# Kernel tuning notes

Measured on AMD Instinct MI355X. Metric: run time of the kernel, lower is better.

The kernel has to match this reference:

```python
import jax, jax.numpy as jnp
import numpy as np
from jax import lax

B, D, N = 1024, 1024, 65536
M, Ks, DS = 8, 256, 128      # key PQ: subvectors, codewords, subvec dim (D/M)
MV, DV = 8, 256              # value PQ: subvectors, subvec dim (OUT/MV)
OUT = MV * DV
K_TOP = 64


def setup_inputs() -> dict:
    key = jax.random.key(0)
    ks = jax.random.split(key, 7)
    x = jax.random.normal(ks[0], (B, D), dtype=jnp.float32)
    # whitening matrix starts as identity in the module; perturb slightly for a non-trivial test
    whitening_matrix = jnp.eye(D, dtype=jnp.float32) + 0.01 * jax.random.normal(ks[1], (D, D), dtype=jnp.float32)
    key_codebooks = jax.random.normal(ks[2], (M, Ks, DS), dtype=jnp.float32)
    value_codebooks = jax.random.normal(ks[3], (MV, Ks, DV), dtype=jnp.float32)
    bias = jnp.zeros((OUT,), dtype=jnp.float32)
    key_codes = jax.random.randint(ks[4], (N, M), 0, Ks, dtype=jnp.int32)
    value_codes = jax.random.randint(ks[5], (N, MV), 0, Ks, dtype=jnp.int32)
    return {
        "x": x,
        "whitening_matrix": whitening_matrix,
        "key_codebooks": key_codebooks,
        "value_codebooks": value_codebooks,
        "bias": bias,
        "key_codes": key_codes,
        "value_codes": value_codes,
        "k": K_TOP,
    }


def reference(x, whitening_matrix, key_codebooks, value_codebooks, bias, key_codes, value_codes, k):
    # 1) whiten the query (module buffer 'whitening_matrix')
    q = x @ whitening_matrix                      # [B, D]
    qs = q.reshape(B, M, DS)                      # [B, M, DS] query subvectors

    # 2) ADC distance tables: squared L2 between each query subvector and each codeword
    #    dt[b, m, c] = ||qs[b,m] - cb[m,c]||^2
    q_sq = jnp.sum(qs * qs, axis=-1)              # [B, M]
    c_sq = jnp.sum(key_codebooks * key_codebooks, axis=-1)  # [M, Ks]
    cross = jnp.einsum("bmd,mcd->bmc", qs, key_codebooks)   # [B, M, Ks]
    dt = q_sq[:, :, None] + c_sq[None, :, :] - 2.0 * cross  # [B, M, Ks]

    # 3) asymmetric distance to all N stored keys via code gather (irregular access)
    lut = dt.transpose(1, 0, 2)                   # [M, B, Ks]
    # per-subvector gather then sum: d[b, n] = sum_m lut[m, b, key_codes[n, m]]
    dists = jax.vmap(lambda l, c: l[:, c])(lut, key_codes.T).sum(axis=0)  # [B, N]

    # 4) top-k nearest neighbors
    neg_top, top_idx = lax.top_k(-dists, k)       # [B, k]

    # 5) reconstruct values of retrieved neighbors from value PQ codebooks
    vc = value_codes[top_idx]                     # [B, k, MV] int codes
    vals = value_codebooks[jnp.arange(MV)[None, None, :], vc]  # [B, k, MV, DV]
    vals = vals.reshape(vals.shape[0], vals.shape[1], OUT)      # [B, k, OUT]

    # 6) distance-weighted aggregation (softmax over negative distances) + bias
    w = jax.nn.softmax(neg_top, axis=-1)          # [B, k]
    y = jnp.einsum("bk,bko->bo", w, vals) + bias  # [B, OUT]
    return y
```

## Files before the change

### kernel.cpp

```cpp
#include <hip/hip_runtime.h>

#define N_ITEMS 65536

__launch_bounds__(256)
__global__ void gemm_q_kernel(const float* __restrict__ A,
                              const float* __restrict__ W,
                              float* __restrict__ qpart) {
  __shared__ float As[16][132];
  __shared__ float Bs[16][132];
  const int tid = threadIdx.x;
  const int tx = tid & 15, ty = tid >> 4;
  const int rb = blockIdx.y * 128, cb = blockIdx.x * 128;
  const int kz = blockIdx.z * 256;
  const int ar = tid >> 2, ac = (tid & 3) << 2;
  const int bk = tid >> 5, bc = (tid & 31) << 2;

  float4 va0 = *(const float4*)&A[(rb + ar) * 1024 + kz + ac];
  float4 va1 = *(const float4*)&A[(rb + ar + 64) * 1024 + kz + ac];
  float4 vb0 = *(const float4*)&W[(kz + bk) * 1024 + cb + bc];
  float4 vb1 = *(const float4*)&W[(kz + bk + 8) * 1024 + cb + bc];

  float acc[8][8] = {};
  for (int k0 = 0; k0 < 256; k0 += 16) {
    As[ac + 0][ar] = va0.x; As[ac + 1][ar] = va0.y;
    As[ac + 2][ar] = va0.z; As[ac + 3][ar] = va0.w;
    As[ac + 0][ar + 64] = va1.x; As[ac + 1][ar + 64] = va1.y;
    As[ac + 2][ar + 64] = va1.z; As[ac + 3][ar + 64] = va1.w;
    *(float4*)&Bs[bk][bc] = vb0;
    *(float4*)&Bs[bk + 8][bc] = vb1;
    __syncthreads();
    if (k0 + 16 < 256) {
      va0 = *(const float4*)&A[(rb + ar) * 1024 + kz + k0 + 16 + ac];
      va1 = *(const float4*)&A[(rb + ar + 64) * 1024 + kz + k0 + 16 + ac];
      vb0 = *(const float4*)&W[(kz + k0 + 16 + bk) * 1024 + cb + bc];
      vb1 = *(const float4*)&W[(kz + k0 + 16 + bk + 8) * 1024 + cb + bc];
    }
#pragma unroll
    for (int kk = 0; kk < 16; kk++) {
      const float4 a0 = *(const float4*)&As[kk][ty << 2];
      const float4 a1 = *(const float4*)&As[kk][64 + (ty << 2)];
      const float4 b0 = *(const float4*)&Bs[kk][tx << 2];
      const float4 b1 = *(const float4*)&Bs[kk][64 + (tx << 2)];
      const float ar8[8] = {a0.x, a0.y, a0.z, a0.w, a1.x, a1.y, a1.z, a1.w};
      const float br8[8] = {b0.x, b0.y, b0.z, b0.w, b1.x, b1.y, b1.z, b1.w};
#pragma unroll
      for (int r = 0; r < 8; r++)
#pragma unroll
        for (int c = 0; c < 8; c++)
          acc[r][c] = fmaf(ar8[r], br8[c], acc[r][c]);
    }
    __syncthreads();
  }
  float* outp = qpart + blockIdx.z * 1048576;
#pragma unroll
  for (int rh = 0; rh < 2; rh++)
#pragma unroll
    for (int r = 0; r < 4; r++) {
      const int row = rb + rh * 64 + (ty << 2) + r;
      const int ri = rh * 4 + r;
      *(float4*)&outp[row * 1024 + cb + (tx << 2)] =
          make_float4(acc[ri][0], acc[ri][1], acc[ri][2], acc[ri][3]);
      *(float4*)&outp[row * 1024 + cb + 64 + (tx << 2)] =
          make_float4(acc[ri][4], acc[ri][5], acc[ri][6], acc[ri][7]);
    }
}

__launch_bounds__(256)
__global__ void lut_kernel(const float* __restrict__ qpart,
                           const float* __restrict__ kcb,
                           const int* __restrict__ key_codes,
                           float* __restrict__ lut,
                           unsigned long long* __restrict__ pcodes,
                           uint4* __restrict__ poffs) {
  if (blockIdx.z == 8) {
    const int g0 = (((int)blockIdx.y * 4 + (int)blockIdx.x) * 256 + (int)threadIdx.x) * 4;
#pragma unroll
    for (int t = 0; t < 4; t++) {
      const int gid = g0 + t;
      unsigned long long p = 0ull;
      unsigned h[8];
#pragma unroll
      for (int j = 0; j < 8; j++) {
        const unsigned c = (unsigned)key_codes[gid * 8 + j] & 255u;
        p |= (unsigned long long)c << (8 * j);
        h[j] = ((c >> 1) << 7) | ((c & 1u) << 2);
      }
      pcodes[gid] = p;
      poffs[gid] = make_uint4(h[0] | (h[1] << 16), h[2] | (h[3] << 16),
                              h[4] | (h[5] << 16), h[6] | (h[7] << 16));
    }
    return;
  }

  __shared__ float As[32][68];
  __shared__ float Bs[32][68];
  const int tid = threadIdx.x;
  const int tx = tid & 15, ty = tid >> 4;
  const int m = blockIdx.z;
  const int rb = blockIdx.y * 64;
  const int cb0 = blockIdx.x * 64;
  float acc[4][4] = {};
  float qa[4] = {}, cs[4] = {};
  for (int k0 = 0; k0 < 128; k0 += 32) {
#pragma unroll
    for (int l = 0; l < 2; l++) {
      const int e = tid + l * 256;
      const int row = e >> 3, c4 = (e & 7) << 2;
      const int qidx = (rb + row) * 1024 + m * 128 + k0 + c4;
      const float4 p0 = *(const float4*)&qpart[qidx];
      const float4 p1 = *(const float4*)&qpart[qidx + 1048576];
      const float4 p2 = *(const float4*)&qpart[qidx + 2097152];
      const float4 p3 = *(const float4*)&qpart[qidx + 3145728];
      const float4 va = make_float4(p0.x + p1.x + p2.x + p3.x,
                                    p0.y + p1.y + p2.y + p3.y,
                                    p0.z + p1.z + p2.z + p3.z,
                                    p0.w + p1.w + p2.w + p3.w);
      As[c4 + 0][row] = va.x; As[c4 + 1][row] = va.y;
      As[c4 + 2][row] = va.z; As[c4 + 3][row] = va.w;
      const float4 vb = *(const float4*)&kcb[(m * 256 + cb0 + row) * 128 + k0 + c4];
      Bs[c4 + 0][row] = vb.x; Bs[c4 + 1][row] = vb.y;
      Bs[c4 + 2][row] = vb.z; Bs[c4 + 3][row] = vb.w;
    }
    __syncthreads();
#pragma unroll
    for (int kk = 0; kk < 32; kk++) {
      const float4 a = *(const float4*)&As[kk][ty << 2];
      const float4 b = *(const float4*)&Bs[kk][tx << 2];
      const float ar[4] = {a.x, a.y, a.z, a.w};
      const float br[4] = {b.x, b.y, b.z, b.w};
#pragma unroll
      for (int r = 0; r < 4; r++)
#pragma unroll
        for (int c = 0; c < 4; c++)
          acc[r][c] = fmaf(ar[r], br[c], acc[r][c]);
#pragma unroll
      for (int r = 0; r < 4; r++) qa[r] = fmaf(ar[r], ar[r], qa[r]);
#pragma unroll
      for (int c = 0; c < 4; c++) cs[c] = fmaf(br[c], br[c], cs[c]);
    }
    __syncthreads();
  }
#pragma unroll
  for (int r = 0; r < 4; r++) {
    const int row = rb + (ty << 2) + r;
    const int col = cb0 + (tx << 2);
    float4 v;
    v.x = qa[r] + cs[0] - 2.0f * acc[r][0];
    v.y = qa[r] + cs[1] - 2.0f * acc[r][1];
    v.z = qa[r] + cs[2] - 2.0f * acc[r][2];
    v.w = qa[r] + cs[3] - 2.0f * acc[r][3];
    *(float4*)&lut[row * 2048 + m * 256 + col] = v;
  }
}

extern __shared__ char dyn_lds[];

__launch_bounds__(1024)
__global__ void scan2r_kernel(const float* __restrict__ lut,
                              const uint4* __restrict__ poffs,
                              unsigned* __restrict__ cand_d,
                              unsigned short* __restrict__ cand_n) {
  char* repb = dyn_lds;
  unsigned* repw = (unsigned*)dyn_lds;
  short* temps = (short*)(dyn_lds + 131072);
  unsigned* tempw = (unsigned*)(dyn_lds + 131072);
  const int tid = threadIdx.x;
  const int g = blockIdx.x;

  {
    const int w = tid >> 6, lane = tid & 63;
    const int rr = w & 1, seg = w >> 1;
    const int row = (g << 1) + rr;
    const int e0 = seg * 256 + lane * 4;
    const float4 v4 = *(const float4*)&lut[row * 2048 + e0];
    float s4 = v4.x + v4.y + v4.z + v4.w;
#pragma unroll
    for (int off = 32; off > 0; off >>= 1) s4 += __shfl_xor(s4, off);
    const float mean = s4 * (1.0f / 256.0f);
    const float vals[4] = {v4.x, v4.y, v4.z, v4.w};
#pragma unroll
    for (int k = 0; k < 4; k++) {
      float f = (vals[k] - mean) * 64.0f;
      f = fmaxf(fminf(f, 32000.0f), -32000.0f);
      temps[(e0 + k) * 2 + rr] = (short)(int)rintf(f);
    }
  }
  __syncthreads();

  {
    const int lane = tid & 63;
    const unsigned v0 = tempw[tid * 2];
    const unsigned v1 = tempw[tid * 2 + 1];
    const int Dbase = tid * 32;
#pragma unroll
    for (int k = 0; k < 16; k++) {
      const int r = (k + lane) & 15;
      repw[Dbase + 2 * r] = v0;
      repw[Dbase + 1 + 2 * r] = v1;
    }
  }
  __syncthreads();

  const int r = tid & 15;
  const char* base0 = repb + (r << 3);
  const char* base1 = repb + 65536 + (r << 3);
  int d0a = 0x7FFFFFFF, d1a = 0x7FFFFFFF, i0a = 0, i1a = 0;
  int d0b = 0x7FFFFFFF, d1b = 0x7FFFFFFF, i0b = 0, i1b = 0;

  uint4 oc = poffs[tid];
  uint4 nc = poffs[tid + 1024];
  for (int it = 0; it < 64; it++) {
    const int n = tid + (it << 10);
    uint4 nn2 = nc;
    if (it < 62) nn2 = poffs[n + 2048];
    unsigned wv;
    int s0, s1;
    wv = *(const unsigned*)(base0 + (oc.x & 0xFFFFu));
    s0 = (int)(short)wv; s1 = ((int)wv) >> 16;
#define LK(B, HV, OFS) { wv = *(const unsigned*)((B) + (HV) + (OFS)); \
    s0 += (int)(short)wv; s1 += ((int)wv) >> 16; }
    LK(base0, oc.x >> 16, 16384)
    LK(base0, oc.y & 0xFFFFu, 32768)
    LK(base0, oc.y >> 16, 49152)
    LK(base1, oc.z & 0xFFFFu, 0)
    LK(base1, oc.z >> 16, 16384)
    LK(base1, oc.w & 0xFFFFu, 32768)
    LK(base1, oc.w >> 16, 49152)
#undef LK
    if (s0 < d1a) {
      if (s0 < d0a) { d1a = d0a; i1a = i0a; d0a = s0; i0a = n; }
      else          { d1a = s0; i1a = n; }
    }
    if (s1 < d1b) {
      if (s1 < d0b) { d1b = d0b; i1b = i0b; d0b = s1; i0b = n; }
      else          { d1b = s1; i1b = n; }
    }
    oc = nc; nc = nn2;
  }

  {
    const int ba = (g << 1) * 2048 + tid * 2;
    *(uint2*)&cand_d[ba] = make_uint2((unsigned)(d0a + 0x40000000),
                                      (unsigned)(d1a + 0x40000000));
    *(unsigned*)&cand_n[ba] = (unsigned)i0a | ((unsigned)i1a << 16);
    const int bb = ((g << 1) + 1) * 2048 + tid * 2;
    *(uint2*)&cand_d[bb] = make_uint2((unsigned)(d0b + 0x40000000),
                                      (unsigned)(d1b + 0x40000000));
    *(unsigned*)&cand_n[bb] = (unsigned)i0b | ((unsigned)i1b << 16);
  }
}

__launch_bounds__(512)
__global__ void scan16_kernel(const float* __restrict__ lut,
                              const unsigned long long* __restrict__ pcodes,
                              unsigned* __restrict__ cand_d,
                              unsigned short* __restrict__ cand_n) {
  __shared__ short sRep[32768];
  const int tid = threadIdx.x;
  const int b = blockIdx.x;

  const float4 v4 = *(const float4*)&lut[b * 2048 + tid * 4];
  float s4 = v4.x + v4.y + v4.z + v4.w;
#pragma unroll
  for (int off = 32; off > 0; off >>= 1) s4 += __shfl_xor(s4, off);
  const float mean = s4 * (1.0f / 256.0f);

  const float vals[4] = {v4.x, v4.y, v4.z, v4.w};
#pragma unroll
  for (int k2 = 0; k2 < 4; k2++) {
    float f = (vals[k2] - mean) * 64.0f;
    f = fmaxf(fminf(f, 32000.0f), -32000.0f);
    const int iv = (int)rintf(f);
    const unsigned hw = (unsigned)(unsigned short)iv;
    const unsigned wrd = hw | (hw << 16);
    const uint4 wv = make_uint4(wrd, wrd, wrd, wrd);
    const int e = tid * 4 + k2;
    *(uint4*)&((unsigned*)sRep)[e * 8] = wv;
    *(uint4*)&((unsigned*)sRep)[e * 8 + 4] = wv;
  }
  __syncthreads();

  const int r = tid & 15;
  int d0 = 0x7FFFFFFF, d1 = 0x7FFFFFFF, d2 = 0x7FFFFFFF, d3 = 0x7FFFFFFF;
  int i0 = 0, i1 = 0, i2 = 0, i3 = 0;

  unsigned long long c8 = pcodes[tid];
  for (int it = 0; it < 128; it++) {
    const int n = tid + (it << 9);
    unsigned long long nxt = 0ull;
    if (it < 127) nxt = pcodes[n + 512];
    const unsigned lo = (unsigned)c8;
    const unsigned hi = (unsigned)(c8 >> 32);
    int s;
    s  = sRep[(((lo      ) & 255u) << 4) + r        ];
    s += sRep[(((lo >>  8) & 255u) << 4) + r +  4096];
    s += sRep[(((lo >> 16) & 255u) << 4) + r +  8192];
    s += sRep[(((lo >> 24)       ) << 4) + r + 12288];
    s += sRep[(((hi      ) & 255u) << 4) + r + 16384];
    s += sRep[(((hi >>  8) & 255u) << 4) + r + 20480];
    s += sRep[(((hi >> 16) & 255u) << 4) + r + 24576];
    s += sRep[(((hi >> 24)       ) << 4) + r + 28672];
    if (s < d3) {
      if (s < d1) {
        if (s < d0) { d3 = d2; i3 = i2; d2 = d1; i2 = i1; d1 = d0; i1 = i0; d0 = s; i0 = n; }
        else        { d3 = d2; i3 = i2; d2 = d1; i2 = i1; d1 = s; i1 = n; }
      } else {
        if (s < d2) { d3 = d2; i3 = i2; d2 = s; i2 = n; }
        else        { d3 = s; i3 = n; }
      }
    }
    c8 = nxt;
  }

  const int base = b * 2048 + tid * 4;
  const uint4 dv = make_uint4((unsigned)(d0 + 0x40000000), (unsigned)(d1 + 0x40000000),
                              (unsigned)(d2 + 0x40000000), (unsigned)(d3 + 0x40000000));
  *(uint4*)&cand_d[base] = dv;
  const unsigned ni01 = (unsigned)i0 | ((unsigned)i1 << 16);
  const unsigned ni23 = (unsigned)i2 | ((unsigned)i3 << 16);
  *(uint2*)&cand_n[base] = make_uint2(ni01, ni23);
}

__launch_bounds__(256)
__global__ void select_kernel(const unsigned* __restrict__ cand_d,
                              const unsigned short* __restrict__ cand_n,
                              const int* __restrict__ value_codes,
                              const float* __restrict__ vcb,
                              const float* __restrict__ bias,
                              float* __restrict__ out) {
  __shared__ unsigned sredw[4];
  __shared__ unsigned long long clist[256];
  __shared__ float sw[256];
  __shared__ int svc[2048];
  __shared__ int scnt;
  __shared__ float sWsum;

  const int tid = threadIdx.x;
  const int b = blockIdx.x;

  const uint4 a0 = *(const uint4*)&cand_d[b * 2048 + tid * 8];
  const uint4 a1 = *(const uint4*)&cand_d[b * 2048 + tid * 8 + 4];
  const uint4 nn = *(const uint4*)&cand_n[b * 2048 + tid * 8];
  unsigned dk[8] = {a0.x, a0.y, a0.z, a0.w, a1.x, a1.y, a1.z, a1.w};
  unsigned ni[8] = {nn.x & 0xFFFFu, nn.x >> 16, nn.y & 0xFFFFu, nn.y >> 16,
                    nn.z & 0xFFFFu, nn.z >> 16, nn.w & 0xFFFFu, nn.w >> 16};

  if (tid == 0) scnt = 0;
  unsigned mn = dk[0];
#pragma unroll
  for (int j = 1; j < 8; j++) mn = (dk[j] < mn) ? dk[j] : mn;
#pragma unroll
  for (int off = 32; off > 0; off >>= 1) {
    const unsigned o = __shfl_xor(mn, off);
    mn = (o < mn) ? o : mn;
  }
  if ((tid & 63) == 0) sredw[tid >> 6] = mn;
  __syncthreads();
  unsigned sMin = sredw[0];
  sMin = (sredw[1] < sMin) ? sredw[1] : sMin;
  sMin = (sredw[2] < sMin) ? sredw[2] : sMin;
  sMin = (sredw[3] < sMin) ? sredw[3] : sMin;
  const unsigned lim = sMin + 2048u;

  const int lane = tid & 63;
  const unsigned long long lm = (1ull << lane) - 1ull;
#pragma unroll
  for (int j = 0; j < 8; j++) {
    const bool pred = dk[j] <= lim;
    const unsigned long long mask = __ballot(pred);
    int base = 0;
    if (lane == 0 && mask) base = atomicAdd(&scnt, __popcll(mask));
    base = __shfl(base, 0);
    if (pred) {
      const int pos = base + __popcll(mask & lm);
      if (pos < 256) clist[pos] = ((unsigned long long)dk[j] << 32) | ni[j];
    }
  }
  __syncthreads();
  const int cnt = min(scnt, 256);

  if (tid < cnt) {
    const int gap = (int)((unsigned)(clist[tid] >> 32)) - (int)sMin;
    sw[tid] = __expf((float)gap * -0.015625f);
  }
  for (int i = tid; i < (cnt << 3); i += 256)
    svc[i] = value_codes[((int)(clist[i >> 3] & 0xFFFFFFFFu)) * 8 + (i & 7)];
  __syncthreads();

  if (tid < 64) {
    float s = 0.f;
    for (int j = tid; j < cnt; j += 64) s += sw[j];
#pragma unroll
    for (int off = 32; off > 0; off >>= 1) s += __shfl_xor(s, off);
    if (tid == 0) sWsum = s;
  }
  __syncthreads();
  const float inv = 1.0f / sWsum;

  const int c0 = tid << 3;
  const int mv = c0 >> 8;
  const int off = c0 & 255;
  float4 acc0 = make_float4(0.f, 0.f, 0.f, 0.f);
  float4 acc1 = make_float4(0.f, 0.f, 0.f, 0.f);
  const float* vbase = vcb + mv * 65536 + off;
  for (int k = 0; k < cnt; k++) {
    const float w = sw[k];
    const float* vp = vbase + svc[(k << 3) + mv] * 256;
    const float4 v0 = *(const float4*)vp;
    const float4 v1 = *(const float4*)(vp + 4);
    acc0.x = fmaf(w, v0.x, acc0.x); acc0.y = fmaf(w, v0.y, acc0.y);
    acc0.z = fmaf(w, v0.z, acc0.z); acc0.w = fmaf(w, v0.w, acc0.w);
    acc1.x = fmaf(w, v1.x, acc1.x); acc1.y = fmaf(w, v1.y, acc1.y);
    acc1.z = fmaf(w, v1.z, acc1.z); acc1.w = fmaf(w, v1.w, acc1.w);
  }
  const float4 b0 = *(const float4*)&bias[c0];
  const float4 b1 = *(const float4*)&bias[c0 + 4];
  *(float4*)&out[b * 2048 + c0] =
      make_float4(fmaf(acc0.x, inv, b0.x), fmaf(acc0.y, inv, b0.y),
                  fmaf(acc0.z, inv, b0.z), fmaf(acc0.w, inv, b0.w));
  *(float4*)&out[b * 2048 + c0 + 4] =
      make_float4(fmaf(acc1.x, inv, b1.x), fmaf(acc1.y, inv, b1.y),
                  fmaf(acc1.z, inv, b1.z), fmaf(acc1.w, inv, b1.w));
}

extern "C" void kernel_launch(void* const* d_in, const int* in_sizes, int n_in,
                              void* d_out, int out_size, void* d_ws, size_t ws_size,
                              hipStream_t stream) {
  const float* x    = (const float*)d_in[0];
  const float* W    = (const float*)d_in[1];
  const float* kcb  = (const float*)d_in[2];
  const float* vcb  = (const float*)d_in[3];
  const float* bias = (const float*)d_in[4];
  const int* key_codes   = (const int*)d_in[5];
  const int* value_codes = (const int*)d_in[6];
  float* out = (float*)d_out;

  float* qpart = (float*)d_ws;
  float* lut   = qpart + 4194304;
  uint4* poffs = (uint4*)(lut + 2097152);
  unsigned long long* pcodes = (unsigned long long*)(poffs + 65536);
  unsigned* cand_d = (unsigned*)d_ws;
  unsigned short* cand_n = (unsigned short*)(cand_d + 2097152);

  hipLaunchKernelGGL(gemm_q_kernel, dim3(8, 8, 4), dim3(256), 0, stream,
                     x, W, qpart);
  hipLaunchKernelGGL(lut_kernel, dim3(4, 16, 9), dim3(256), 0, stream,
                     qpart, kcb, key_codes, lut, pcodes, poffs);

  const hipError_t attr_rc = hipFuncSetAttribute(
      (const void*)scan2r_kernel, hipFuncAttributeMaxDynamicSharedMemorySize, 139264);
  if (attr_rc == hipSuccess) {
    hipLaunchKernelGGL(scan2r_kernel, dim3(512), dim3(1024), 139264, stream,
                       lut, poffs, cand_d, cand_n);
  } else {
    hipLaunchKernelGGL(scan16_kernel, dim3(1024), dim3(512), 0, stream,
                       lut, pcodes, cand_d, cand_n);
  }

  hipLaunchKernelGGL(select_kernel, dim3(1024), dim3(256), 0, stream,
                     cand_d, cand_n, value_codes, vcb, bias, out);
}
```

Before: 197.4 us.

## Shrink GEMM tiles to 64x64 single-wave blocks and move code packing into GEMM launch

The whitening GEMM now uses 64-thread blocks on 64x64 output tiles, so a 16x16x4 grid launches 1024 blocks instead of 256 to fill more compute units. The key-code packing work moves from the LUT kernel's extra z-slice into an extra z-slice of the GEMM launch, so it runs alongside the GEMM. The LUT kernel loses those blocks. Smaller tiles lower operand reuse per block and raise global and LDS traffic per flop.

```diff
diff --git a/kernel.cpp b/kernel.cpp
--- a/kernel.cpp
+++ b/kernel.cpp
@@ -2,78 +2,15 @@
 
 #define N_ITEMS 65536
 
-__launch_bounds__(256)
+__launch_bounds__(64)
 __global__ void gemm_q_kernel(const float* __restrict__ A,
                               const float* __restrict__ W,
-                              float* __restrict__ qpart) {
-  __shared__ float As[16][132];
-  __shared__ float Bs[16][132];
-  const int tid = threadIdx.x;
-  const int tx = tid & 15, ty = tid >> 4;
-  const int rb = blockIdx.y * 128, cb = blockIdx.x * 128;
-  const int kz = blockIdx.z * 256;
-  const int ar = tid >> 2, ac = (tid & 3) << 2;
-  const int bk = tid >> 5, bc = (tid & 31) << 2;
-
-  float4 va0 = *(const float4*)&A[(rb + ar) * 1024 + kz + ac];
-  float4 va1 = *(const float4*)&A[(rb + ar + 64) * 1024 + kz + ac];
-  float4 vb0 = *(const float4*)&W[(kz + bk) * 1024 + cb + bc];
-  float4 vb1 = *(const float4*)&W[(kz + bk + 8) * 1024 + cb + bc];
-
-  float acc[8][8] = {};
-  for (int k0 = 0; k0 < 256; k0 += 16) {
-    As[ac + 0][ar] = va0.x; As[ac + 1][ar] = va0.y;
-    As[ac + 2][ar] = va0.z; As[ac + 3][ar] = va0.w;
-    As[ac + 0][ar + 64] = va1.x; As[ac + 1][ar + 64] = va1.y;
-    As[ac + 2][ar + 64] = va1.z; As[ac + 3][ar + 64] = va1.w;
-    *(float4*)&Bs[bk][bc] = vb0;
-    *(float4*)&Bs[bk + 8][bc] = vb1;
-    __syncthreads();
-    if (k0 + 16 < 256) {
-      va0 = *(const float4*)&A[(rb + ar) * 1024 + kz + k0 + 16 + ac];
-      va1 = *(const float4*)&A[(rb + ar + 64) * 1024 + kz + k0 + 16 + ac];
-      vb0 = *(const float4*)&W[(kz + k0 + 16 + bk) * 1024 + cb + bc];
-      vb1 = *(const float4*)&W[(kz + k0 + 16 + bk + 8) * 1024 + cb + bc];
-    }
-#pragma unroll
-    for (int kk = 0; kk < 16; kk++) {
-      const float4 a0 = *(const float4*)&As[kk][ty << 2];
-      const float4 a1 = *(const float4*)&As[kk][64 + (ty << 2)];
-      const float4 b0 = *(const float4*)&Bs[kk][tx << 2];
-      const float4 b1 = *(const float4*)&Bs[kk][64 + (tx << 2)];
-      const float ar8[8] = {a0.x, a0.y, a0.z, a0.w, a1.x, a1.y, a1.z, a1.w};
-      const float br8[8] = {b0.x, b0.y, b0.z, b0.w, b1.x, b1.y, b1.z, b1.w};
-#pragma unroll
-      for (int r = 0; r < 8; r++)
-#pragma unroll
-        for (int c = 0; c < 8; c++)
-          acc[r][c] = fmaf(ar8[r], br8[c], acc[r][c]);
-    }
-    __syncthreads();
-  }
-  float* outp = qpart + blockIdx.z * 1048576;
-#pragma unroll
-  for (int rh = 0; rh < 2; rh++)
-#pragma unroll
-    for (int r = 0; r < 4; r++) {
-      const int row = rb + rh * 64 + (ty << 2) + r;
-      const int ri = rh * 4 + r;
-      *(float4*)&outp[row * 1024 + cb + (tx << 2)] =
-          make_float4(acc[ri][0], acc[ri][1], acc[ri][2], acc[ri][3]);
-      *(float4*)&outp[row * 1024 + cb + 64 + (tx << 2)] =
-          make_float4(acc[ri][4], acc[ri][5], acc[ri][6], acc[ri][7]);
-    }
-}
-
-__launch_bounds__(256)
-__global__ void lut_kernel(const float* __restrict__ qpart,
-                           const float* __restrict__ kcb,
-                           const int* __restrict__ key_codes,
-                           float* __restrict__ lut,
-                           unsigned long long* __restrict__ pcodes,
-                           uint4* __restrict__ poffs) {
-  if (blockIdx.z == 8) {
-    const int g0 = (((int)blockIdx.y * 4 + (int)blockIdx.x) * 256 + (int)threadIdx.x) * 4;
+                              float* __restrict__ qpart,
+                              const int* __restrict__ key_codes,
+                              unsigned long long* __restrict__ pcodes,
+                              uint4* __restrict__ poffs) {
+  if (blockIdx.z == 4) {
+    const int g0 = (((int)blockIdx.y * 16 + (int)blockIdx.x) * 64 + (int)threadIdx.x) * 4;
 #pragma unroll
     for (int t = 0; t < 4; t++) {
       const int gid = g0 + t;
@@ -92,6 +29,74 @@
     return;
   }
 
+  __shared__ float As[16][68];
+  __shared__ float Bs[16][68];
+  const int tid = threadIdx.x;
+  const int tx = tid & 7, ty = tid >> 3;
+  const int rb = blockIdx.y * 64, cb = blockIdx.x * 64;
+  const int kz = blockIdx.z * 256;
+
+  float4 va[4], vb[4];
+#pragma unroll
+  for (int j = 0; j < 4; j++) {
+    const int e = tid + (j << 6);
+    va[j] = *(const float4*)&A[(rb + (e >> 2)) * 1024 + kz + ((e & 3) << 2)];
+    vb[j] = *(const float4*)&W[(kz + (e >> 4)) * 1024 + cb + ((e & 15) << 2)];
+  }
+
+  float acc[8][8] = {};
+  for (int k0 = 0; k0 < 256; k0 += 16) {
+#pragma unroll
+    for (int j = 0; j < 4; j++) {
+      const int e = tid + (j << 6);
+      const int row = e >> 2, c4 = (e & 3) << 2;
+      As[c4 + 0][row] = va[j].x; As[c4 + 1][row] = va[j].y;
+      As[c4 + 2][row] = va[j].z; As[c4 + 3][row] = va[j].w;
+      *(float4*)&Bs[e >> 4][(e & 15) << 2] = vb[j];
+    }
+    __syncthreads();
+    if (k0 + 16 < 256) {
+#pragma unroll
+      for (int j = 0; j < 4; j++) {
+        const int e = tid + (j << 6);
+        va[j] = *(const float4*)&A[(rb + (e >> 2)) * 1024 + kz + k0 + 16 + ((e & 3) << 2)];
+        vb[j] = *(const float4*)&W[(kz + k0 + 16 + (e >> 4)) * 1024 + cb + ((e & 15) << 2)];
+      }
+    }
+#pragma unroll
+    for (int kk = 0; kk < 16; kk++) {
+      const float4 a0 = *(const float4*)&As[kk][ty << 2];
+      const float4 a1 = *(const float4*)&As[kk][32 + (ty << 2)];
+      const float4 b0 = *(const float4*)&Bs[kk][tx << 2];
+      const float4 b1 = *(const float4*)&Bs[kk][32 + (tx << 2)];
+      const float ar8[8] = {a0.x, a0.y, a0.z, a0.w, a1.x, a1.y, a1.z, a1.w};
+      const float br8[8] = {b0.x, b0.y, b0.z, b0.w, b1.x, b1.y, b1.z, b1.w};
+#pragma unroll
+      for (int r = 0; r < 8; r++)
+#pragma unroll
+        for (int c = 0; c < 8; c++)
+          acc[r][c] = fmaf(ar8[r], br8[c], acc[r][c]);
+    }
+    __syncthreads();
+  }
+  float* outp = qpart + blockIdx.z * 1048576;
+#pragma unroll
+  for (int rh = 0; rh < 2; rh++)
+#pragma unroll
+    for (int r = 0; r < 4; r++) {
+      const int row = rb + rh * 32 + (ty << 2) + r;
+      const int ri = rh * 4 + r;
+      *(float4*)&outp[row * 1024 + cb + (tx << 2)] =
+          make_float4(acc[ri][0], acc[ri][1], acc[ri][2], acc[ri][3]);
+      *(float4*)&outp[row * 1024 + cb + 32 + (tx << 2)] =
+          make_float4(acc[ri][4], acc[ri][5], acc[ri][6], acc[ri][7]);
+    }
+}
+
+__launch_bounds__(256)
+__global__ void lut_kernel(const float* __restrict__ qpart,
+                           const float* __restrict__ kcb,
+                           float* __restrict__ lut) {
   __shared__ float As[32][68];
   __shared__ float Bs[32][68];
   const int tid = threadIdx.x;
@@ -442,10 +447,10 @@
   unsigned* cand_d = (unsigned*)d_ws;
   unsigned short* cand_n = (unsigned short*)(cand_d + 2097152);
 
-  hipLaunchKernelGGL(gemm_q_kernel, dim3(8, 8, 4), dim3(256), 0, stream,
-                     x, W, qpart);
-  hipLaunchKernelGGL(lut_kernel, dim3(4, 16, 9), dim3(256), 0, stream,
-                     qpart, kcb, key_codes, lut, pcodes, poffs);
+  hipLaunchKernelGGL(gemm_q_kernel, dim3(16, 16, 5), dim3(64), 0, stream,
+                     x, W, qpart, key_codes, pcodes, poffs);
+  hipLaunchKernelGGL(lut_kernel, dim3(4, 16, 8), dim3(256), 0, stream,
+                     qpart, kcb, lut);
 
   const hipError_t attr_rc = hipFuncSetAttribute(
       (const void*)scan2r_kernel, hipFuncAttributeMaxDynamicSharedMemorySize, 139264);
```

Result: slower. 212.3 us (+7.6%).
